# Optimization experiments

Measured on AMD Instinct MI355X. Metric: run time of the kernel, lower is better.

The kernel has to match this reference:

```python
import jax, jax.numpy as jnp
import numpy as np

N_NODES = 100000


def setup_inputs() -> dict:
    key = jax.random.key(0)
    ks = jax.random.split(key, 8)
    E = 1600000
    x = jax.random.normal(ks[0], (N_NODES, 128), dtype=jnp.float32)
    src = jax.random.randint(ks[1], (E,), 0, N_NODES, dtype=jnp.int32)
    dst = jax.random.randint(ks[2], (E,), 0, N_NODES, dtype=jnp.int32)
    s = 1.0 / np.sqrt(128.0)
    w_self = jax.random.normal(ks[3], (5, 128, 128), dtype=jnp.float32) * s
    w_neigh = jax.random.normal(ks[4], (5, 128, 128), dtype=jnp.float32) * s
    b = jnp.zeros((5, 128), dtype=jnp.float32)
    w_self_out = jax.random.normal(ks[5], (128, 47), dtype=jnp.float32) * s
    w_neigh_out = jax.random.normal(ks[6], (128, 47), dtype=jnp.float32) * s
    b_out = jnp.zeros((47,), dtype=jnp.float32)
    return {"x": x, "src": src, "dst": dst, "w_self": w_self, "w_neigh": w_neigh,
            "b": b, "w_self_out": w_self_out, "w_neigh_out": w_neigh_out, "b_out": b_out}


def _mean_agg(h, src, dst, inv_deg):
    # segment-sum of source features into destination nodes, then mean
    summed = jax.ops.segment_sum(h[src], dst, num_segments=N_NODES)  # [N, d]
    return summed * inv_deg[:, None]


def _sage_layer(h, src, dst, inv_deg, ws, wn, bias):
    neigh = _mean_agg(h, src, dst, inv_deg)
    return h @ ws + neigh @ wn + bias


def reference(x, src, dst, w_self, w_neigh, b, w_self_out, w_neigh_out, b_out):
    # in-degree, clamped to 1 for isolated nodes (DGL mean aggregator behavior)
    deg = jax.ops.segment_sum(jnp.ones_like(dst, dtype=x.dtype), dst, num_segments=N_NODES)
    inv_deg = 1.0 / jnp.maximum(deg, 1.0)

    # layer 0: no ReLU after (matches original forward)
    h = _sage_layer(x, src, dst, inv_deg, w_self[0], w_neigh[0], b[0])
    # layers 1..4: SAGEConv + ReLU
    for i in range(1, 5):
        h = _sage_layer(h, src, dst, inv_deg, w_self[i], w_neigh[i], b[i])
        h = jax.nn.relu(h)
    # final layer: 128 -> num_classes, no activation
    h = _sage_layer(h, src, dst, inv_deg, w_self_out, w_neigh_out, b_out)
    return h
```

## Files before the change

### kernel.cpp

```cpp
#include <hip/hip_runtime.h>

typedef float f4 __attribute__((ext_vector_type(4)));
typedef float f32x4 __attribute__((ext_vector_type(4)));
typedef float f2 __attribute__((ext_vector_type(2)));
typedef short s16x8 __attribute__((ext_vector_type(8)));
typedef int i4 __attribute__((ext_vector_type(4)));

#define N_NODES 100000
#define NBUCK 196
#define NB1 256

__device__ inline unsigned short f2bf(float f) {
    unsigned int u = __builtin_bit_cast(unsigned int, f);
    u += 0x7FFFu + ((u >> 16) & 1u);
    return (unsigned short)(u >> 16);
}
__device__ inline float bflo(unsigned int v) { return __builtin_bit_cast(float, v << 16); }
__device__ inline float bfhi(unsigned int v) { return __builtin_bit_cast(float, v & 0xFFFF0000u); }


__global__ __launch_bounds__(256) void k_hist(const int* __restrict__ dst,
                                              int* __restrict__ histG, int E) {
    __shared__ int h[NBUCK];
    int tid = threadIdx.x;
    for (int i = tid; i < NBUCK; i += 256) h[i] = 0;
    __syncthreads();
    int chunk = (E + NB1 - 1) / NB1;
    int s = blockIdx.x * chunk, eN = min(E, s + chunk);
    for (int i = s + tid; i < eN; i += 256) atomicAdd(&h[dst[i] >> 9], 1);
    __syncthreads();
    for (int i = tid; i < NBUCK; i += 256) histG[i * NB1 + blockIdx.x] = h[i];
}

__global__ __launch_bounds__(1024) void k_scanB(int* __restrict__ histG) {
    __shared__ int ps[1024];
    int t = threadIdx.x;
    int base = t * 49;
    int vals[49];
    int sum = 0;
#pragma unroll
    for (int i = 0; i < 49; ++i) { vals[i] = histG[base + i]; sum += vals[i]; }
    ps[t] = sum;
    __syncthreads();
    for (int off = 1; off < 1024; off <<= 1) {
        int v = (t >= off) ? ps[t - off] : 0;
        __syncthreads();
        ps[t] += v;
        __syncthreads();
    }
    int run = ps[t] - sum;
#pragma unroll
    for (int i = 0; i < 49; ++i) { int v = vals[i]; histG[base + i] = run; run += v; }
}

__global__ __launch_bounds__(256) void k_place(const int* __restrict__ src,
                                               const int* __restrict__ dst,
                                               const int* __restrict__ histG,
                                               unsigned int* __restrict__ ebuf, int E) {
    __shared__ int cur[NBUCK];
    int tid = threadIdx.x;
    for (int i = tid; i < NBUCK; i += 256) cur[i] = histG[i * NB1 + blockIdx.x];
    __syncthreads();
    int chunk = (E + NB1 - 1) / NB1;
    int s = blockIdx.x * chunk, eN = min(E, s + chunk);
    for (int i = s + tid; i < eN; i += 256) {
        int d = dst[i];
        int b = d >> 9;
        int pos = atomicAdd(&cur[b], 1);
        ebuf[pos] = (unsigned int)src[i] | ((unsigned int)(d & 511) << 17);
    }
}

__global__ __launch_bounds__(256) void k_csr(const unsigned int* __restrict__ ebuf,
                                             const int* __restrict__ histG,
                                             int* __restrict__ rp, int* __restrict__ col,
                                             float* __restrict__ invd, int N, int E) {
    __shared__ int ldeg[512];
    __shared__ int lbase[512];
    int b = blockIdx.x, tid = threadIdx.x;
    int base = histG[b * NB1];
    int endB = (b == NBUCK - 1) ? E : histG[(b + 1) * NB1];
    int cnt = endB - base;
    int n0 = b << 9;

    ldeg[tid] = 0;
    ldeg[tid + 256] = 0;
    __syncthreads();
    for (int i = tid; i < cnt; i += 256) atomicAdd(&ldeg[ebuf[base + i] >> 17], 1);
    __syncthreads();

    int a0 = ldeg[tid], a1 = ldeg[tid + 256];
    lbase[tid] = a0;
    lbase[tid + 256] = a1;
    __syncthreads();
    for (int off = 1; off < 512; off <<= 1) {
        int v0 = (tid >= off) ? lbase[tid - off] : 0;
        int v1 = (tid + 256 >= off) ? lbase[tid + 256 - off] : 0;
        __syncthreads();
        lbase[tid] += v0;
        lbase[tid + 256] += v1;
        __syncthreads();
    }
    int e0 = lbase[tid] - a0, e1 = lbase[tid + 256] - a1;
    __syncthreads();
    lbase[tid] = e0;
    lbase[tid + 256] = e1;
    ldeg[tid] = 0;
    ldeg[tid + 256] = 0;
    __syncthreads();

    for (int i = tid; i < cnt; i += 256) {
        unsigned int p = ebuf[base + i];
        int dl = p >> 17;
        int pos = base + lbase[dl] + atomicAdd(&ldeg[dl], 1);
        col[pos] = (int)(p & 0x1FFFFu) << 8;
    }

    int g0 = n0 + tid, g1 = n0 + tid + 256;
    if (g0 < N) { rp[g0] = base + e0; invd[g0] = 1.0f / fmaxf((float)a0, 1.0f); }
    if (g1 < N) { rp[g1] = base + e1; invd[g1] = 1.0f / fmaxf((float)a1, 1.0f); }
    if (b == NBUCK - 1 && tid == 0) rp[N] = E;
    if (b == NBUCK - 1 && tid < 32) col[E + tid] = 0;
}


__global__ void k_cvt(const float* __restrict__ x, unsigned short* __restrict__ xb, int n8) {
    int t = blockIdx.x * 256 + threadIdx.x;
    if (t >= n8) return;
    f4 a = *(const f4*)&x[(size_t)t * 8];
    f4 b = *(const f4*)&x[(size_t)t * 8 + 4];
    s16x8 p;
    p[0] = (short)f2bf(a[0]); p[1] = (short)f2bf(a[1]);
    p[2] = (short)f2bf(a[2]); p[3] = (short)f2bf(a[3]);
    p[4] = (short)f2bf(b[0]); p[5] = (short)f2bf(b[1]);
    p[6] = (short)f2bf(b[2]); p[7] = (short)f2bf(b[3]);
    *(s16x8*)&xb[(size_t)t * 8] = p;
}

__global__ void k_prepw(const float* __restrict__ ws, const float* __restrict__ wn,
                        unsigned short* __restrict__ wp) {
    int t = blockIdx.x * 256 + threadIdx.x;
    if (t >= 5 * 4096) return;
    int l = t & 63, nfg = (t >> 6) & 7, ks = (t >> 9) & 7, lyr = t >> 12;
    int n = nfg * 16 + (l & 15);
    s16x8 p;
#pragma unroll
    for (int j = 0; j < 8; ++j) {
        int k = ks * 32 + (l >> 4) * 8 + j;
        float v = (k < 128) ? ws[((size_t)lyr * 128 + k) * 128 + n]
                            : wn[((size_t)lyr * 128 + (k - 128)) * 128 + n];
        p[j] = (short)f2bf(v);
    }
    *(s16x8*)&wp[(size_t)t * 8] = p;
}

__global__ void k_prepwo(const float* __restrict__ wso, const float* __restrict__ wno,
                         unsigned short* __restrict__ wS, unsigned short* __restrict__ wN,
                         const float* __restrict__ bo, float* __restrict__ bo48) {
    int t = blockIdx.x * 256 + threadIdx.x;
    if (t < 48) bo48[t] = (t < 47) ? bo[t] : 0.f;
    if (t >= 2 * 768) return;
    int tbl = t / 768, r = t % 768;
    int ks = r / 192, nf = (r / 64) % 3, l = r & 63;
    int n = nf * 16 + (l & 15);
    const float* W = tbl ? wno : wso;
    unsigned short* dstp = tbl ? wN : wS;
    s16x8 p;
#pragma unroll
    for (int j = 0; j < 8; ++j) {
        int k = ks * 32 + (l >> 4) * 8 + j;
        float v = (n < 47) ? W[(size_t)k * 47 + n] : 0.f;
        p[j] = (short)f2bf(v);
    }
    *(s16x8*)&dstp[(size_t)r * 8] = p;
}


__global__ __launch_bounds__(256) void k_agg(const unsigned short* __restrict__ h,
                                             const int* __restrict__ rp,
                                             const int* __restrict__ col,
                                             const float* __restrict__ invd,
                                             unsigned short* __restrict__ out, int n) {
    int gw = (blockIdx.x * 256 + threadIdx.x) >> 6;
    int lane = threadIdx.x & 63;
    if (gw >= n) return;
    const char* hb = (const char*)h;
    const int lb = lane * 4;
    int beg = rp[gw], end = rp[gw + 1];
    f2 acc = {0.f, 0.f};
    int e = beg;
    for (; e + 8 <= end; e += 8) {
        i4 c0, c1;
        __builtin_memcpy(&c0, &col[e], 16);
        __builtin_memcpy(&c1, &col[e + 4], 16);
        unsigned int u[8];
#pragma unroll
        for (int i = 0; i < 4; ++i)
            u[i] = *(const unsigned int*)(hb + (unsigned int)(c0[i] + lb));
#pragma unroll
        for (int i = 0; i < 4; ++i)
            u[4 + i] = *(const unsigned int*)(hb + (unsigned int)(c1[i] + lb));
#pragma unroll
        for (int i = 0; i < 8; ++i) {
            f2 v = {bflo(u[i]), bfhi(u[i])};
            acc += v;
        }
    }
    if (e < end) {
        int rem = end - e;
        i4 c0, c1;
        __builtin_memcpy(&c0, &col[e], 16);
        __builtin_memcpy(&c1, &col[e + 4], 16);
        unsigned int u[8];
#pragma unroll
        for (int i = 0; i < 4; ++i)
            u[i] = *(const unsigned int*)(hb + (unsigned int)(c0[i] + lb));
#pragma unroll
        for (int i = 0; i < 4; ++i)
            u[4 + i] = *(const unsigned int*)(hb + (unsigned int)(c1[i] + lb));
#pragma unroll
        for (int i = 0; i < 8; ++i) {
            if (i < rem) {
                f2 v = {bflo(u[i]), bfhi(u[i])};
                acc += v;
            }
        }
    }
    float iv = invd[gw];
    unsigned int r = (unsigned int)f2bf(acc[0] * iv) | ((unsigned int)f2bf(acc[1] * iv) << 16);
    ((unsigned int*)out)[(size_t)gw * 64 + lane] = r;
}


__global__ __launch_bounds__(256) void gemm128d(const unsigned short* __restrict__ h,
                                                const unsigned short* __restrict__ nb,
                                                const unsigned short* __restrict__ wl,
                                                const float* __restrict__ bias,
                                                unsigned short* __restrict__ out,
                                                int M, int relu) {
    const int tid = threadIdx.x;
    const int l = tid & 63, wv = tid >> 6;
    const int mh = wv >> 1, nh = wv & 1;
    const int r0 = blockIdx.x * 64;
    const s16x8* wf = (const s16x8*)wl;
    const int cgb = (l >> 4) << 3;

    int R[2];
#pragma unroll
    for (int mf = 0; mf < 2; ++mf) {
        int r = r0 + mh * 32 + mf * 16 + (l & 15);
        R[mf] = (r > M - 1) ? (M - 1) : r;
    }

    f32x4 acc[2][4];
#pragma unroll
    for (int i = 0; i < 2; ++i)
#pragma unroll
        for (int j = 0; j < 4; ++j) acc[i][j] = (f32x4)0.f;

#pragma unroll
    for (int ks = 0; ks < 8; ++ks) {
        const unsigned short* A = (ks < 4) ? h : nb;
        const int kk = ks & 3;
        s16x8 ha[2];
#pragma unroll
        for (int mf = 0; mf < 2; ++mf)
            ha[mf] = *(const s16x8*)(A + (size_t)R[mf] * 128 + kk * 32 + cgb);
#pragma unroll
        for (int nf = 0; nf < 4; ++nf) {
            s16x8 bw = wf[(ks * 8 + nh * 4 + nf) * 64 + l];
            acc[0][nf] = __builtin_amdgcn_mfma_f32_16x16x32_bf16(bw, ha[0], acc[0][nf], 0, 0, 0);
            acc[1][nf] = __builtin_amdgcn_mfma_f32_16x16x32_bf16(bw, ha[1], acc[1][nf], 0, 0, 0);
        }
    }

    f4 bv[4];
#pragma unroll
    for (int nf = 0; nf < 4; ++nf)
        bv[nf] = *(const f4*)&bias[nh * 64 + nf * 16 + ((l >> 4) << 2)];

#pragma unroll
    for (int mf = 0; mf < 2; ++mf) {
        int row = r0 + mh * 32 + mf * 16 + (l & 15);
        if (row >= M) continue;
#pragma unroll
        for (int nf = 0; nf < 4; ++nf) {
            int ncol = nh * 64 + nf * 16 + ((l >> 4) << 2);
            f32x4 a = acc[mf][nf];
            float v0 = a[0] + bv[nf][0], v1 = a[1] + bv[nf][1];
            float v2 = a[2] + bv[nf][2], v3 = a[3] + bv[nf][3];
            if (relu) {
                v0 = fmaxf(v0, 0.f); v1 = fmaxf(v1, 0.f);
                v2 = fmaxf(v2, 0.f); v3 = fmaxf(v3, 0.f);
            }
            uint2 p;
            p.x = (unsigned int)f2bf(v0) | ((unsigned int)f2bf(v1) << 16);
            p.y = (unsigned int)f2bf(v2) | ((unsigned int)f2bf(v3) << 16);
            *(uint2*)(out + (size_t)row * 128 + ncol) = p;
        }
    }
}


__global__ __launch_bounds__(256) void gemm_fin(const unsigned short* __restrict__ h,
                                                const unsigned short* __restrict__ wS,
                                                const unsigned short* __restrict__ wN,
                                                const float* __restrict__ bo48,
                                                unsigned short* __restrict__ tmpn,
                                                float* __restrict__ selfo, int M) {
    const int tid = threadIdx.x;
    const int l = tid & 63, wv = tid >> 6;
    const int mh = wv >> 1, sel = wv & 1;
    const int r0 = blockIdx.x * 64;
    const s16x8* wf = (const s16x8*)(sel ? wN : wS);
    const int cgb = (l >> 4) << 3;

    int R[2];
#pragma unroll
    for (int mf = 0; mf < 2; ++mf) {
        int r = r0 + mh * 32 + mf * 16 + (l & 15);
        R[mf] = (r > M - 1) ? (M - 1) : r;
    }

    f32x4 acc[2][3];
#pragma unroll
    for (int i = 0; i < 2; ++i)
#pragma unroll
        for (int j = 0; j < 3; ++j) acc[i][j] = (f32x4)0.f;

#pragma unroll
    for (int ks = 0; ks < 4; ++ks) {
        s16x8 ha[2];
#pragma unroll
        for (int mf = 0; mf < 2; ++mf)
            ha[mf] = *(const s16x8*)(h + (size_t)R[mf] * 128 + ks * 32 + cgb);
#pragma unroll
        for (int nf = 0; nf < 3; ++nf) {
            s16x8 bw = wf[(ks * 3 + nf) * 64 + l];
            acc[0][nf] = __builtin_amdgcn_mfma_f32_16x16x32_bf16(bw, ha[0], acc[0][nf], 0, 0, 0);
            acc[1][nf] = __builtin_amdgcn_mfma_f32_16x16x32_bf16(bw, ha[1], acc[1][nf], 0, 0, 0);
        }
    }

#pragma unroll
    for (int mf = 0; mf < 2; ++mf) {
        int row = r0 + mh * 32 + mf * 16 + (l & 15);
        if (row >= M) continue;
#pragma unroll
        for (int nf = 0; nf < 3; ++nf) {
            int ncol = nf * 16 + ((l >> 4) << 2);
            f32x4 a = acc[mf][nf];
            if (sel == 0) {
                f4 bv = *(const f4*)&bo48[ncol];
                f4 o;
                o[0] = a[0] + bv[0]; o[1] = a[1] + bv[1];
                o[2] = a[2] + bv[2]; o[3] = a[3] + bv[3];
                *(f4*)&selfo[(size_t)row * 48 + ncol] = o;
            } else {
                uint2 p;
                p.x = (unsigned int)f2bf(a[0]) | ((unsigned int)f2bf(a[1]) << 16);
                p.y = (unsigned int)f2bf(a[2]) | ((unsigned int)f2bf(a[3]) << 16);
                *(uint2*)(tmpn + (size_t)row * 64 + ncol) = p;
            }
        }
    }
}


__global__ __launch_bounds__(256) void k_agg_fin(const unsigned short* __restrict__ z,
                                                 const float* __restrict__ selfo,
                                                 const int* __restrict__ rp,
                                                 const int* __restrict__ col,
                                                 const float* __restrict__ invd,
                                                 float* __restrict__ out, int n) {
    int gw = (blockIdx.x * 256 + threadIdx.x) >> 6;
    int lane = threadIdx.x & 63;
    if (gw >= n) return;
    const char* zb = (const char*)z;
    const int hhalf = lane >> 5;
    const int lb = (lane & 31) * 4;
    int beg = rp[gw], end = rp[gw + 1];
    f2 acc = {0.f, 0.f};
    int e = beg;
    for (; e + 8 <= end; e += 8) {
        unsigned int u[4];
#pragma unroll
        for (int j = 0; j < 4; ++j) {
            unsigned int c = (unsigned int)col[e + 2 * j + hhalf];
            u[j] = *(const unsigned int*)(zb + (c >> 1) + lb);
        }
#pragma unroll
        for (int j = 0; j < 4; ++j) { f2 v = {bflo(u[j]), bfhi(u[j])}; acc += v; }
    }
    if (e < end) {
        int rem = end - e;
        unsigned int u[4];
#pragma unroll
        for (int j = 0; j < 4; ++j) {
            unsigned int c = (unsigned int)col[e + 2 * j + hhalf];
            u[j] = *(const unsigned int*)(zb + (c >> 1) + lb);
        }
#pragma unroll
        for (int j = 0; j < 4; ++j) {
            if (2 * j + hhalf < rem) { f2 v = {bflo(u[j]), bfhi(u[j])}; acc += v; }
        }
    }
    f2 tot;
    tot[0] = acc[0] + __shfl_xor(acc[0], 32);
    tot[1] = acc[1] + __shfl_xor(acc[1], 32);
    float iv = invd[gw];
    if (lane < 24) {
        int c0 = lane * 2;
        f2 s = *(const f2*)&selfo[(size_t)gw * 48 + c0];
        out[(size_t)gw * 47 + c0] = s[0] + tot[0] * iv;
        if (c0 + 1 < 47) out[(size_t)gw * 47 + c0 + 1] = s[1] + tot[1] * iv;
    }
}


static inline char* alignp(char* p) {
    return (char*)(((size_t)p + 255) & ~(size_t)255);
}

extern "C" void kernel_launch(void* const* d_in, const int* in_sizes, int n_in,
                              void* d_out, int out_size, void* d_ws, size_t ws_size,
                              hipStream_t stream) {
    const float* x = (const float*)d_in[0];
    const int* src = (const int*)d_in[1];
    const int* dst = (const int*)d_in[2];
    const float* w_self = (const float*)d_in[3];
    const float* w_neigh = (const float*)d_in[4];
    const float* b = (const float*)d_in[5];
    const float* wso = (const float*)d_in[6];
    const float* wno = (const float*)d_in[7];
    const float* bo = (const float*)d_in[8];
    float* out = (float*)d_out;

    const int N = N_NODES;
    const int E = in_sizes[1];

    char* w = (char*)d_ws;
    unsigned short* xb = (unsigned short*)w;   w = alignp(w + (size_t)N * 128 * 2);
    unsigned short* hA = (unsigned short*)w;   w = alignp(w + (size_t)N * 128 * 2);
    unsigned short* hB = (unsigned short*)w;   w = alignp(w + (size_t)N * 128 * 2);
    unsigned short* nbuf = (unsigned short*)w; w = alignp(w + (size_t)N * 128 * 2);
    unsigned short* wp = (unsigned short*)w;   w = alignp(w + (size_t)5 * 32768 * 2);
    unsigned short* wS = (unsigned short*)w;   w = alignp(w + (size_t)768 * 8 * 2);
    unsigned short* wN = (unsigned short*)w;   w = alignp(w + (size_t)768 * 8 * 2);
    float* bo48 = (float*)w; w = alignp(w + 48 * 4);
    int* rp = (int*)w;       w = alignp(w + (size_t)(N + 4) * 4);
    int* col = (int*)w;      w = alignp(w + (size_t)(E + 32) * 4);
    int* histG = (int*)w;    w = alignp(w + (size_t)NBUCK * NB1 * 4);
    float* invd = (float*)w; w = alignp(w + (size_t)N * 4);

    unsigned int* ebuf = (unsigned int*)hB;
    unsigned short* tmpn = nbuf;

    k_hist<<<NB1, 256, 0, stream>>>(dst, histG, E);
    k_scanB<<<1, 1024, 0, stream>>>(histG);
    k_place<<<NB1, 256, 0, stream>>>(src, dst, histG, ebuf, E);
    k_csr<<<NBUCK, 256, 0, stream>>>(ebuf, histG, rp, col, invd, N, E);

    k_cvt<<<(N * 128 / 8 + 255) / 256, 256, 0, stream>>>(x, xb, N * 128 / 8);
    k_prepw<<<(5 * 4096 + 255) / 256, 256, 0, stream>>>(w_self, w_neigh, wp);
    k_prepwo<<<6, 256, 0, stream>>>(wso, wno, wS, wN, bo, bo48);

    const int aggBlocks = (N * 64 + 255) / 256;
    const int gemmBlocks = (N + 63) / 64;

    k_agg<<<aggBlocks, 256, 0, stream>>>(xb, rp, col, invd, nbuf, N);
    gemm128d<<<gemmBlocks, 256, 0, stream>>>(xb, nbuf, wp, b, hA, N, 0);

    unsigned short* cur = hA;
    unsigned short* oth = hB;
    for (int lyr = 1; lyr < 5; ++lyr) {
        k_agg<<<aggBlocks, 256, 0, stream>>>(cur, rp, col, invd, nbuf, N);
        gemm128d<<<gemmBlocks, 256, 0, stream>>>(cur, nbuf, wp + (size_t)lyr * 32768,
                                                 b + (size_t)lyr * 128, oth, N, 1);
        unsigned short* t = cur; cur = oth; oth = t;
    }

    float* selfo = (float*)hB;
    gemm_fin<<<gemmBlocks, 256, 0, stream>>>(cur, wS, wN, bo48, tmpn, selfo, N);
    k_agg_fin<<<aggBlocks, 256, 0, stream>>>(tmpn, selfo, rp, col, invd, out, N);
}
```

Before: 578.9 us.

## Split aggregation into feature halves and stage GEMM A tiles in LDS

The aggregation kernel now splits each node's 128 features into two halves handled by separate blocks. Each wave processes two edges at once, one per 32-lane half, and the halves are combined with a cross-lane shuffle. This is meant to keep the gathered feature working set smaller for cache locality and to raise memory-level parallelism. The layer GEMM now uses 128-row tiles with self and neighbour inputs staged in shared memory, doubling weight reuse per fragment load at the cost of 64KB of LDS per block, which lowers occupancy.

```diff
diff --git a/kernel.cpp b/kernel.cpp
--- a/kernel.cpp
+++ b/kernel.cpp
@@ -176,102 +176,116 @@
 }
 
 
-__global__ __launch_bounds__(256) void k_agg(const unsigned short* __restrict__ h,
-                                             const int* __restrict__ rp,
-                                             const int* __restrict__ col,
-                                             const float* __restrict__ invd,
-                                             unsigned short* __restrict__ out, int n) {
-    int gw = (blockIdx.x * 256 + threadIdx.x) >> 6;
-    int lane = threadIdx.x & 63;
-    if (gw >= n) return;
-    const char* hb = (const char*)h;
-    const int lb = lane * 4;
-    int beg = rp[gw], end = rp[gw + 1];
+__global__ __launch_bounds__(256) void k_agg_h(const unsigned short* __restrict__ h,
+                                               const int* __restrict__ rp,
+                                               const int* __restrict__ col,
+                                               const float* __restrict__ invd,
+                                               unsigned short* __restrict__ out, int n) {
+    const int bid = blockIdx.x;
+    const int half = bid & 1;
+    const int node = (bid >> 1) * 4 + (threadIdx.x >> 6);
+    const int lane = threadIdx.x & 63;
+    if (node >= n) return;
+    const char* hb = (const char*)h + half * 128;
+    const int lb = (lane & 31) * 4;
+    const int hl = lane >> 5;
+    int beg = rp[node], end = rp[node + 1];
     f2 acc = {0.f, 0.f};
     int e = beg;
-    for (; e + 8 <= end; e += 8) {
-        i4 c0, c1;
-        __builtin_memcpy(&c0, &col[e], 16);
-        __builtin_memcpy(&c1, &col[e + 4], 16);
+    for (; e + 16 <= end; e += 16) {
         unsigned int u[8];
 #pragma unroll
-        for (int i = 0; i < 4; ++i)
-            u[i] = *(const unsigned int*)(hb + (unsigned int)(c0[i] + lb));
-#pragma unroll
-        for (int i = 0; i < 4; ++i)
-            u[4 + i] = *(const unsigned int*)(hb + (unsigned int)(c1[i] + lb));
-#pragma unroll
-        for (int i = 0; i < 8; ++i) {
-            f2 v = {bflo(u[i]), bfhi(u[i])};
-            acc += v;
-        }
+        for (int j = 0; j < 8; ++j) {
+            unsigned int c = (unsigned int)col[e + 2 * j + hl];
+            u[j] = *(const unsigned int*)(hb + c + lb);
+        }
+#pragma unroll
+        for (int j = 0; j < 8; ++j) { f2 v = {bflo(u[j]), bfhi(u[j])}; acc += v; }
+    }
+    if (e + 8 <= end) {
+        unsigned int u[4];
+#pragma unroll
+        for (int j = 0; j < 4; ++j) {
+            unsigned int c = (unsigned int)col[e + 2 * j + hl];
+            u[j] = *(const unsigned int*)(hb + c + lb);
+        }
+#pragma unroll
+        for (int j = 0; j < 4; ++j) { f2 v = {bflo(u[j]), bfhi(u[j])}; acc += v; }
+        e += 8;
     }
     if (e < end) {
         int rem = end - e;
-        i4 c0, c1;
-        __builtin_memcpy(&c0, &col[e], 16);
-        __builtin_memcpy(&c1, &col[e + 4], 16);
-        unsigned int u[8];
-#pragma unroll
-        for (int i = 0; i < 4; ++i)
-            u[i] = *(const unsigned int*)(hb + (unsigned int)(c0[i] + lb));
-#pragma unroll
-        for (int i = 0; i < 4; ++i)
-            u[4 + i] = *(const unsigned int*)(hb + (unsigned int)(c1[i] + lb));
-#pragma unroll
-        for (int i = 0; i < 8; ++i) {
-            if (i < rem) {
-                f2 v = {bflo(u[i]), bfhi(u[i])};
-                acc += v;
-            }
-        }
-    }
-    float iv = invd[gw];
-    unsigned int r = (unsigned int)f2bf(acc[0] * iv) | ((unsigned int)f2bf(acc[1] * iv) << 16);
-    ((unsigned int*)out)[(size_t)gw * 64 + lane] = r;
-}
-
-
-__global__ __launch_bounds__(256) void gemm128d(const unsigned short* __restrict__ h,
-                                                const unsigned short* __restrict__ nb,
-                                                const unsigned short* __restrict__ wl,
-                                                const float* __restrict__ bias,
-                                                unsigned short* __restrict__ out,
-                                                int M, int relu) {
+        unsigned int u[4];
+#pragma unroll
+        for (int j = 0; j < 4; ++j) {
+            unsigned int c = (unsigned int)col[e + 2 * j + hl];
+            u[j] = *(const unsigned int*)(hb + c + lb);
+        }
+#pragma unroll
+        for (int j = 0; j < 4; ++j) {
+            if (2 * j + hl < rem) { f2 v = {bflo(u[j]), bfhi(u[j])}; acc += v; }
+        }
+    }
+    f2 tot;
+    tot[0] = acc[0] + __shfl_xor(acc[0], 32);
+    tot[1] = acc[1] + __shfl_xor(acc[1], 32);
+    if (lane < 32) {
+        float iv = invd[node];
+        unsigned int r = (unsigned int)f2bf(tot[0] * iv) | ((unsigned int)f2bf(tot[1] * iv) << 16);
+        ((unsigned int*)out)[(size_t)node * 64 + half * 32 + lane] = r;
+    }
+}
+
+
+__global__ __launch_bounds__(256) void gemm128(const unsigned short* __restrict__ h,
+                                               const unsigned short* __restrict__ nb,
+                                               const unsigned short* __restrict__ wl,
+                                               const float* __restrict__ bias,
+                                               unsigned short* __restrict__ out,
+                                               int M, int relu) {
+    __shared__ s16x8 afr[4096];
     const int tid = threadIdx.x;
-    const int l = tid & 63, wv = tid >> 6;
-    const int mh = wv >> 1, nh = wv & 1;
-    const int r0 = blockIdx.x * 64;
+    const int l = tid & 63, w = tid >> 6;
+    const int r0 = blockIdx.x * 128;
+    const int cg = (w * 4 + (l >> 4)) * 8;
+
+    s16x8 th[8], tn[8];
+#pragma unroll
+    for (int i = 0; i < 8; ++i) {
+        int r = r0 + i * 16 + (l & 15);
+        if (r >= M) r = M - 1;
+        th[i] = *(const s16x8*)(h + (size_t)r * 128 + cg);
+        tn[i] = *(const s16x8*)(nb + (size_t)r * 128 + cg);
+    }
+#pragma unroll
+    for (int i = 0; i < 8; ++i) {
+        afr[(w * 8 + i) * 64 + l] = th[i];
+        afr[((w + 4) * 8 + i) * 64 + l] = tn[i];
+    }
+    __syncthreads();
+
+    const int mh = w >> 1, nh = w & 1;
     const s16x8* wf = (const s16x8*)wl;
-    const int cgb = (l >> 4) << 3;
-
-    int R[2];
-#pragma unroll
-    for (int mf = 0; mf < 2; ++mf) {
-        int r = r0 + mh * 32 + mf * 16 + (l & 15);
-        R[mf] = (r > M - 1) ? (M - 1) : r;
-    }
-
-    f32x4 acc[2][4];
-#pragma unroll
-    for (int i = 0; i < 2; ++i)
+
+    f32x4 acc[4][4];
+#pragma unroll
+    for (int i = 0; i < 4; ++i)
 #pragma unroll
         for (int j = 0; j < 4; ++j) acc[i][j] = (f32x4)0.f;
 
 #pragma unroll
     for (int ks = 0; ks < 8; ++ks) {
-        const unsigned short* A = (ks < 4) ? h : nb;
-        const int kk = ks & 3;
-        s16x8 ha[2];
-#pragma unroll
-        for (int mf = 0; mf < 2; ++mf)
-            ha[mf] = *(const s16x8*)(A + (size_t)R[mf] * 128 + kk * 32 + cgb);
-#pragma unroll
-        for (int nf = 0; nf < 4; ++nf) {
-            s16x8 bw = wf[(ks * 8 + nh * 4 + nf) * 64 + l];
-            acc[0][nf] = __builtin_amdgcn_mfma_f32_16x16x32_bf16(bw, ha[0], acc[0][nf], 0, 0, 0);
-            acc[1][nf] = __builtin_amdgcn_mfma_f32_16x16x32_bf16(bw, ha[1], acc[1][nf], 0, 0, 0);
-        }
+        s16x8 bw[4], ha[4];
+#pragma unroll
+        for (int nf = 0; nf < 4; ++nf) bw[nf] = wf[(ks * 8 + nh * 4 + nf) * 64 + l];
+#pragma unroll
+        for (int mf = 0; mf < 4; ++mf) ha[mf] = afr[(ks * 8 + mh * 4 + mf) * 64 + l];
+#pragma unroll
+        for (int mf = 0; mf < 4; ++mf)
+#pragma unroll
+            for (int nf = 0; nf < 4; ++nf)
+                acc[mf][nf] = __builtin_amdgcn_mfma_f32_16x16x32_bf16(bw[nf], ha[mf],
+                                                                      acc[mf][nf], 0, 0, 0);
     }
 
     f4 bv[4];
@@ -280,8 +294,8 @@
         bv[nf] = *(const f4*)&bias[nh * 64 + nf * 16 + ((l >> 4) << 2)];
 
 #pragma unroll
-    for (int mf = 0; mf < 2; ++mf) {
-        int row = r0 + mh * 32 + mf * 16 + (l & 15);
+    for (int mf = 0; mf < 4; ++mf) {
+        int row = r0 + mh * 64 + mf * 16 + (l & 15);
         if (row >= M) continue;
 #pragma unroll
         for (int nf = 0; nf < 4; ++nf) {
@@ -465,22 +479,24 @@
     k_prepw<<<(5 * 4096 + 255) / 256, 256, 0, stream>>>(w_self, w_neigh, wp);
     k_prepwo<<<6, 256, 0, stream>>>(wso, wno, wS, wN, bo, bo48);
 
-    const int aggBlocks = (N * 64 + 255) / 256;
-    const int gemmBlocks = (N + 63) / 64;
-
-    k_agg<<<aggBlocks, 256, 0, stream>>>(xb, rp, col, invd, nbuf, N);
-    gemm128d<<<gemmBlocks, 256, 0, stream>>>(xb, nbuf, wp, b, hA, N, 0);
+    const int aggBlocks = 2 * ((N + 3) / 4);
+    const int aggFinBlocks = (N * 64 + 255) / 256;
+    const int gemmBlocks = (N + 127) / 128;
+    const int finBlocks = (N + 63) / 64;
+
+    k_agg_h<<<aggBlocks, 256, 0, stream>>>(xb, rp, col, invd, nbuf, N);
+    gemm128<<<gemmBlocks, 256, 0, stream>>>(xb, nbuf, wp, b, hA, N, 0);
 
     unsigned short* cur = hA;
     unsigned short* oth = hB;
     for (int lyr = 1; lyr < 5; ++lyr) {
-        k_agg<<<aggBlocks, 256, 0, stream>>>(cur, rp, col, invd, nbuf, N);
-        gemm128d<<<gemmBlocks, 256, 0, stream>>>(cur, nbuf, wp + (size_t)lyr * 32768,
-                                                 b + (size_t)lyr * 128, oth, N, 1);
+        k_agg_h<<<aggBlocks, 256, 0, stream>>>(cur, rp, col, invd, nbuf, N);
+        gemm128<<<gemmBlocks, 256, 0, stream>>>(cur, nbuf, wp + (size_t)lyr * 32768,
+                                                b + (size_t)lyr * 128, oth, N, 1);
         unsigned short* t = cur; cur = oth; oth = t;
     }
 
     float* selfo = (float*)hB;
-    gemm_fin<<<gemmBlocks, 256, 0, stream>>>(cur, wS, wN, bo48, tmpn, selfo, N);
-    k_agg_fin<<<aggBlocks, 256, 0, stream>>>(tmpn, selfo, rp, col, invd, out, N);
-}
+    gemm_fin<<<finBlocks, 256, 0, stream>>>(cur, wS, wN, bo48, tmpn, selfo, N);
+    k_agg_fin<<<aggFinBlocks, 256, 0, stream>>>(tmpn, selfo, rp, col, invd, out, N);
+}
```

New measurement: 841.6 us. +45.4%, slower.

## Stage GEMM A tiles in LDS via global_load_lds and enlarge tile to 128 rows

Applied to the files above, without the earlier changes.

The per-layer 128-wide GEMM now loads its A operands (self and neighbour features) directly into shared memory with global_load_lds, then reads them back as MFMA fragments. Each block now covers 128 rows instead of 64, and each wave computes a 4x4 grid of 16x16 fragments, so every weight fragment loaded is reused across more rows. The aim is fewer redundant weight loads and fewer scattered per-lane global reads. The cost is 64KB of LDS per block, which lowers occupancy, and a full wait-for-load barrier before any compute with no overlap.

```diff
diff --git a/kernel.cpp b/kernel.cpp
--- a/kernel.cpp
+++ b/kernel.cpp
@@ -17,6 +17,11 @@
 }
 __device__ inline float bflo(unsigned int v) { return __builtin_bit_cast(float, v << 16); }
 __device__ inline float bfhi(unsigned int v) { return __builtin_bit_cast(float, v & 0xFFFF0000u); }
+
+#define GLDS(gp, lp)                                                            \
+    __builtin_amdgcn_global_load_lds(                                           \
+        (const __attribute__((address_space(1))) void*)(gp),                    \
+        (__attribute__((address_space(3))) void*)(lp), 16, 0, 0)
 
 
 __global__ __launch_bounds__(256) void k_hist(const int* __restrict__ dst,
@@ -232,46 +237,50 @@
 }
 
 
-__global__ __launch_bounds__(256) void gemm128d(const unsigned short* __restrict__ h,
-                                                const unsigned short* __restrict__ nb,
-                                                const unsigned short* __restrict__ wl,
-                                                const float* __restrict__ bias,
-                                                unsigned short* __restrict__ out,
-                                                int M, int relu) {
+__global__ __launch_bounds__(256) void gemm128(const unsigned short* __restrict__ h,
+                                               const unsigned short* __restrict__ nb,
+                                               const unsigned short* __restrict__ wl,
+                                               const float* __restrict__ bias,
+                                               unsigned short* __restrict__ out,
+                                               int M, int relu) {
+    __shared__ s16x8 afr[4096];
     const int tid = threadIdx.x;
-    const int l = tid & 63, wv = tid >> 6;
-    const int mh = wv >> 1, nh = wv & 1;
-    const int r0 = blockIdx.x * 64;
+    const int l = tid & 63, w = tid >> 6;
+    const int r0 = blockIdx.x * 128;
+    const int cg = (w * 4 + (l >> 4)) * 8;
+
+#pragma unroll
+    for (int i = 0; i < 8; ++i) {
+        int r = r0 + i * 16 + (l & 15);
+        if (r >= M) r = M - 1;
+        GLDS(h + (size_t)r * 128 + cg, &afr[(w * 8 + i) * 64]);
+        GLDS(nb + (size_t)r * 128 + cg, &afr[((w + 4) * 8 + i) * 64]);
+    }
+    asm volatile("s_waitcnt vmcnt(0)");
+    __syncthreads();
+
+    const int mh = w >> 1, nh = w & 1;
     const s16x8* wf = (const s16x8*)wl;
-    const int cgb = (l >> 4) << 3;
-
-    int R[2];
-#pragma unroll
-    for (int mf = 0; mf < 2; ++mf) {
-        int r = r0 + mh * 32 + mf * 16 + (l & 15);
-        R[mf] = (r > M - 1) ? (M - 1) : r;
-    }
-
-    f32x4 acc[2][4];
-#pragma unroll
-    for (int i = 0; i < 2; ++i)
+
+    f32x4 acc[4][4];
+#pragma unroll
+    for (int i = 0; i < 4; ++i)
 #pragma unroll
         for (int j = 0; j < 4; ++j) acc[i][j] = (f32x4)0.f;
 
 #pragma unroll
     for (int ks = 0; ks < 8; ++ks) {
-        const unsigned short* A = (ks < 4) ? h : nb;
-        const int kk = ks & 3;
-        s16x8 ha[2];
-#pragma unroll
-        for (int mf = 0; mf < 2; ++mf)
-            ha[mf] = *(const s16x8*)(A + (size_t)R[mf] * 128 + kk * 32 + cgb);
-#pragma unroll
-        for (int nf = 0; nf < 4; ++nf) {
-            s16x8 bw = wf[(ks * 8 + nh * 4 + nf) * 64 + l];
-            acc[0][nf] = __builtin_amdgcn_mfma_f32_16x16x32_bf16(bw, ha[0], acc[0][nf], 0, 0, 0);
-            acc[1][nf] = __builtin_amdgcn_mfma_f32_16x16x32_bf16(bw, ha[1], acc[1][nf], 0, 0, 0);
-        }
+        s16x8 bw[4], ha[4];
+#pragma unroll
+        for (int nf = 0; nf < 4; ++nf) bw[nf] = wf[(ks * 8 + nh * 4 + nf) * 64 + l];
+#pragma unroll
+        for (int mf = 0; mf < 4; ++mf) ha[mf] = afr[(ks * 8 + mh * 4 + mf) * 64 + l];
+#pragma unroll
+        for (int mf = 0; mf < 4; ++mf)
+#pragma unroll
+            for (int nf = 0; nf < 4; ++nf)
+                acc[mf][nf] = __builtin_amdgcn_mfma_f32_16x16x32_bf16(bw[nf], ha[mf],
+                                                                      acc[mf][nf], 0, 0, 0);
     }
 
     f4 bv[4];
@@ -280,8 +289,8 @@
         bv[nf] = *(const f4*)&bias[nh * 64 + nf * 16 + ((l >> 4) << 2)];
 
 #pragma unroll
-    for (int mf = 0; mf < 2; ++mf) {
-        int row = r0 + mh * 32 + mf * 16 + (l & 15);
+    for (int mf = 0; mf < 4; ++mf) {
+        int row = r0 + mh * 64 + mf * 16 + (l & 15);
         if (row >= M) continue;
 #pragma unroll
         for (int nf = 0; nf < 4; ++nf) {
@@ -466,21 +475,22 @@
     k_prepwo<<<6, 256, 0, stream>>>(wso, wno, wS, wN, bo, bo48);
 
     const int aggBlocks = (N * 64 + 255) / 256;
-    const int gemmBlocks = (N + 63) / 64;
+    const int gemmBlocks = (N + 127) / 128;
+    const int finBlocks = (N + 63) / 64;
 
     k_agg<<<aggBlocks, 256, 0, stream>>>(xb, rp, col, invd, nbuf, N);
-    gemm128d<<<gemmBlocks, 256, 0, stream>>>(xb, nbuf, wp, b, hA, N, 0);
+    gemm128<<<gemmBlocks, 256, 0, stream>>>(xb, nbuf, wp, b, hA, N, 0);
 
     unsigned short* cur = hA;
     unsigned short* oth = hB;
     for (int lyr = 1; lyr < 5; ++lyr) {
         k_agg<<<aggBlocks, 256, 0, stream>>>(cur, rp, col, invd, nbuf, N);
-        gemm128d<<<gemmBlocks, 256, 0, stream>>>(cur, nbuf, wp + (size_t)lyr * 32768,
-                                                 b + (size_t)lyr * 128, oth, N, 1);
+        gemm128<<<gemmBlocks, 256, 0, stream>>>(cur, nbuf, wp + (size_t)lyr * 32768,
+                                                b + (size_t)lyr * 128, oth, N, 1);
         unsigned short* t = cur; cur = oth; oth = t;
     }
 
     float* selfo = (float*)hB;
-    gemm_fin<<<gemmBlocks, 256, 0, stream>>>(cur, wS, wN, bo48, tmpn, selfo, N);
+    gemm_fin<<<finBlocks, 256, 0, stream>>>(cur, wS, wN, bo48, tmpn, selfo, N);
     k_agg_fin<<<aggBlocks, 256, 0, stream>>>(tmpn, selfo, rp, col, invd, out, N);
 }
```

Measured after the change: 560.0 us. 1.03x faster.
